# Optimization experiments

Measured on AMD Instinct MI355X. Metric: run time of the kernel, lower is better.

The kernel has to match this reference:

```python
import jax, jax.numpy as jnp
import numpy as np

B, S, H = 32, 2048, 1024

def setup_inputs() -> dict:
    key = jax.random.key(0)
    ks = jax.random.split(key, 8)
    scale = 1.0 / np.sqrt(H)
    return {
        "decoder_hidden": jax.random.normal(ks[0], (B, 1, H), dtype=jnp.float32),
        "encoder_outputs": jax.random.normal(ks[1], (B, S, H), dtype=jnp.float32),
        "coverage": jax.random.uniform(ks[2], (B, S), dtype=jnp.float32),
        "W_enc": jax.random.normal(ks[3], (H, H), dtype=jnp.float32) * scale,  # enc_v.weight [out,in]
        "W_dec": jax.random.normal(ks[4], (H, H), dtype=jnp.float32) * scale,  # dec_v.weight
        "b_dec": jax.random.normal(ks[5], (H,), dtype=jnp.float32) * scale,    # dec_v.bias
        "w_cov": jax.random.normal(ks[6], (H,), dtype=jnp.float32) * scale,    # cov_v.weight [H,1] squeezed
        "v": jax.random.normal(ks[7], (H,), dtype=jnp.float32) * scale,        # V_prime.weight [1,H] squeezed
    }

def reference(decoder_hidden, encoder_outputs, coverage, W_enc, W_dec, b_dec, w_cov, v):
    # enc_feature: [B,S,H]; torch Linear is x @ W.T
    enc_feature = jnp.einsum("bsh,oh->bso", encoder_outputs, W_enc)
    # dec_feature: [B,1,H], broadcasts over S
    dec_feature = jnp.einsum("bqh,oh->bqo", decoder_hidden, W_dec) + b_dec
    # cov_feature: coverage[...,None] @ w_cov[None,:] -> [B,S,H]
    cov_feature = coverage[..., None] * w_cov
    scores = jnp.tanh(enc_feature + dec_feature + cov_feature)  # [B,S,H]
    attn_scores = jnp.einsum("bsh,h->bs", scores, v)            # V_prime, squeeze(-1)
    attn_dist = jax.nn.softmax(attn_scores, axis=-1)[:, None, :]  # [B,1,S]
    return attn_dist
```

## Files before the change

### kernel.cpp

```cpp
#include <hip/hip_runtime.h>
#include <hip/hip_bf16.h>

#define Bb 32
#define Ss 2048
#define Hh 1024

typedef __attribute__((ext_vector_type(4))) float f32x4;
typedef __attribute__((ext_vector_type(8))) short s16x8;

#define GAS const __attribute__((address_space(1))) unsigned int
#define LAS __attribute__((address_space(3))) unsigned int

__device__ __forceinline__ unsigned short f2bf(float x) {
  unsigned int u = __float_as_uint(x);
  u = (u + 0x7fffu + ((u >> 16) & 1u)) >> 16;
  return (unsigned short)u;
}

__global__ void cvt_bf16_kernel(const float* __restrict__ in,
                                unsigned short* __restrict__ out, int n8) {
  int idx = blockIdx.x * blockDim.x + threadIdx.x;
  int stride = gridDim.x * blockDim.x;
  for (int i = idx; i < n8; i += stride) {
    const float4* p = reinterpret_cast<const float4*>(in) + 2 * (size_t)i;
    float4 a = p[0];
    float4 b = p[1];
    union { unsigned short u[8]; uint4 q; } r;
    r.u[0] = f2bf(a.x); r.u[1] = f2bf(a.y); r.u[2] = f2bf(a.z); r.u[3] = f2bf(a.w);
    r.u[4] = f2bf(b.x); r.u[5] = f2bf(b.y); r.u[6] = f2bf(b.z); r.u[7] = f2bf(b.w);
    reinterpret_cast<uint4*>(out)[i] = r.q;
  }
}

__global__ void dec_feat_kernel(const float* __restrict__ dh,
                                const float* __restrict__ Wd,
                                const float* __restrict__ bd,
                                float* __restrict__ out) {
  int gw = blockIdx.x * 4 + (threadIdx.x >> 6);
  int lane = threadIdx.x & 63;
  int b = gw >> 10;
  int o = gw & 1023;
  const float4* x = reinterpret_cast<const float4*>(dh + (size_t)b * Hh);
  const float4* w = reinterpret_cast<const float4*>(Wd + (size_t)o * Hh);
  float acc = 0.f;
#pragma unroll
  for (int it = 0; it < 4; ++it) {
    float4 xa = x[lane + it * 64];
    float4 wa = w[lane + it * 64];
    acc += xa.x * wa.x + xa.y * wa.y + xa.z * wa.z + xa.w * wa.w;
  }
#pragma unroll
  for (int m = 1; m < 64; m <<= 1) acc += __shfl_xor(acc, m, 64);
  if (lane == 0) out[gw] = acc + bd[o];
}

__global__ void __launch_bounds__(256, 2)
gemm_tanh_kernel(const unsigned short* __restrict__ A,
                 const unsigned short* __restrict__ W,
                 const float* __restrict__ decf,
                 const float* __restrict__ cov,
                 const float* __restrict__ wcov,
                 const float* __restrict__ v,
                 float* __restrict__ scores) {
  __shared__ unsigned short lds[2 * 8192];

  int bid = blockIdx.x;
  int swz = (bid & 7) * 512 + (bid >> 3);
  int s_tile = swz >> 3;
  int o_tile = swz & 7;

  const int tid = threadIdx.x;
  const int lane = tid & 63;
  const int wid = tid >> 6;
  const int wr = wid >> 1;
  const int wc = wid & 1;
  const int fr = lane & 15;
  const int fk = (lane >> 4) * 8;

  const size_t a_base = (size_t)s_tile * 128 * 1024;
  const size_t b_base = (size_t)o_tile * 128 * 1024;
  const int st_row = tid >> 2;
  const int st_k = (tid & 3) * 8;
  const unsigned short* gA = A + a_base + (size_t)st_row * 1024 + st_k;
  const unsigned short* gB = W + b_base + (size_t)st_row * 1024 + st_k;
  unsigned short* la = lds + tid * 8;

#define STAGE(buf, kt) do {                                                        \
    const unsigned short* _ga = gA + (size_t)(kt) * 32;                            \
    const unsigned short* _gb = gB + (size_t)(kt) * 32;                            \
    unsigned short* _la = la + (buf) * 8192;                                       \
    __builtin_amdgcn_global_load_lds((GAS*)(_ga),         (LAS*)(_la),        16, 0, 0); \
    __builtin_amdgcn_global_load_lds((GAS*)(_ga + 65536), (LAS*)(_la + 2048), 16, 0, 0); \
    __builtin_amdgcn_global_load_lds((GAS*)(_gb),         (LAS*)(_la + 4096), 16, 0, 0); \
    __builtin_amdgcn_global_load_lds((GAS*)(_gb + 65536), (LAS*)(_la + 6144), 16, 0, 0); \
  } while (0)

  f32x4 acc[4][4];
#pragma unroll
  for (int i = 0; i < 4; ++i)
#pragma unroll
    for (int j = 0; j < 4; ++j) acc[i][j] = (f32x4){0.f, 0.f, 0.f, 0.f};

  STAGE(0, 0);
  __syncthreads();
  int buf = 0;
  const unsigned short* baseA0 = lds + (size_t)(wr * 64 + fr) * 32 + fk;
  const unsigned short* baseB0 = lds + 4096 + (size_t)(wc * 64 + fr) * 32 + fk;

  for (int kt = 0; kt < 32; ++kt) {
    if (kt < 31) STAGE(buf ^ 1, kt + 1);
    const unsigned short* bA = baseA0 + buf * 8192;
    const unsigned short* bB = baseB0 + buf * 8192;
    s16x8 af[4], bfr[4];
#pragma unroll
    for (int i = 0; i < 4; ++i) af[i] = *reinterpret_cast<const s16x8*>(bA + i * 512);
#pragma unroll
    for (int j = 0; j < 4; ++j) bfr[j] = *reinterpret_cast<const s16x8*>(bB + j * 512);
#pragma unroll
    for (int i = 0; i < 4; ++i)
#pragma unroll
      for (int j = 0; j < 4; ++j)
        acc[i][j] = __builtin_amdgcn_mfma_f32_16x16x32_bf16(af[i], bfr[j], acc[i][j], 0, 0, 0);
    __syncthreads();
    buf ^= 1;
  }
#undef STAGE

  const int row_base = s_tile * 128 + wr * 64 + (lane >> 4) * 4;
  const int o_base_g = o_tile * 128 + wc * 64 + fr;
  const int bb = (s_tile * 128) >> 11;

  float vv[4], dv[4], wv[4];
#pragma unroll
  for (int j = 0; j < 4; ++j) {
    int o = o_base_g + j * 16;
    vv[j] = v[o];
    wv[j] = wcov[o];
    dv[j] = decf[bb * 1024 + o];
  }

#pragma unroll
  for (int i = 0; i < 4; ++i) {
#pragma unroll
    for (int r = 0; r < 4; ++r) {
      int s_flat = row_base + i * 16 + r;
      float c = cov[s_flat];
      float sum = 0.f;
#pragma unroll
      for (int j = 0; j < 4; ++j) {
        float x = acc[i][j][r] + dv[j] + c * wv[j];
        sum += tanhf(x) * vv[j];
      }
      sum += __shfl_xor(sum, 1, 64);
      sum += __shfl_xor(sum, 2, 64);
      sum += __shfl_xor(sum, 4, 64);
      sum += __shfl_xor(sum, 8, 64);
      if (fr == 0) atomicAdd(&scores[s_flat], sum);
    }
  }
}

__global__ void softmax_kernel(const float* __restrict__ scores, float* __restrict__ out) {
  int b = blockIdx.x;
  int tid = threadIdx.x;
  int lane = tid & 63, w = tid >> 6;
  const float* row = scores + (size_t)b * Ss;
  float vals[8];
#pragma unroll
  for (int k = 0; k < 8; ++k) vals[k] = row[tid + k * 256];
  float m = vals[0];
#pragma unroll
  for (int k = 1; k < 8; ++k) m = fmaxf(m, vals[k]);
#pragma unroll
  for (int off = 1; off < 64; off <<= 1) m = fmaxf(m, __shfl_xor(m, off, 64));
  __shared__ float sm[4], ss[4];
  if (lane == 0) sm[w] = m;
  __syncthreads();
  m = fmaxf(fmaxf(sm[0], sm[1]), fmaxf(sm[2], sm[3]));
  float s = 0.f;
#pragma unroll
  for (int k = 0; k < 8; ++k) { vals[k] = __expf(vals[k] - m); s += vals[k]; }
#pragma unroll
  for (int off = 1; off < 64; off <<= 1) s += __shfl_xor(s, off, 64);
  if (lane == 0) ss[w] = s;
  __syncthreads();
  s = ss[0] + ss[1] + ss[2] + ss[3];
  float inv = 1.f / s;
#pragma unroll
  for (int k = 0; k < 8; ++k) out[(size_t)b * Ss + tid + k * 256] = vals[k] * inv;
}

extern "C" void kernel_launch(void* const* d_in, const int* in_sizes, int n_in,
                              void* d_out, int out_size, void* d_ws, size_t ws_size,
                              hipStream_t stream) {
  const float* dh    = (const float*)d_in[0];
  const float* enc   = (const float*)d_in[1];
  const float* cov   = (const float*)d_in[2];
  const float* W_enc = (const float*)d_in[3];
  const float* W_dec = (const float*)d_in[4];
  const float* b_dec = (const float*)d_in[5];
  const float* w_cov = (const float*)d_in[6];
  const float* v     = (const float*)d_in[7];
  float* out = (float*)d_out;

  char* ws = (char*)d_ws;
  unsigned short* A_bf  = (unsigned short*)ws;
  unsigned short* W_bf  = (unsigned short*)(ws + 134217728);
  float*          decf  = (float*)(ws + 136314880);
  float*          score = (float*)(ws + 136445952);

  hipMemsetAsync(score, 0, (size_t)Bb * Ss * sizeof(float), stream);
  cvt_bf16_kernel<<<4096, 256, 0, stream>>>(enc, A_bf, (Bb * Ss * Hh) / 8);
  cvt_bf16_kernel<<<512, 256, 0, stream>>>(W_enc, W_bf, (Hh * Hh) / 8);
  dec_feat_kernel<<<(Bb * Hh) / 4, 256, 0, stream>>>(dh, W_dec, b_dec, decf);
  gemm_tanh_kernel<<<4096, 256, 0, stream>>>(A_bf, W_bf, decf, cov, w_cov, v, score);
  softmax_kernel<<<Bb, 256, 0, stream>>>(score, out);
}
```

Before: 282.4 us.

## Fuse fp32-to-bf16 activation conversion into GEMM with larger swizzled tiles

```diff
diff --git a/kernel.cpp b/kernel.cpp
--- a/kernel.cpp
+++ b/kernel.cpp
@@ -17,19 +17,18 @@
   return (unsigned short)u;
 }
 
-__global__ void cvt_bf16_kernel(const float* __restrict__ in,
-                                unsigned short* __restrict__ out, int n8) {
-  int idx = blockIdx.x * blockDim.x + threadIdx.x;
-  int stride = gridDim.x * blockDim.x;
-  for (int i = idx; i < n8; i += stride) {
-    const float4* p = reinterpret_cast<const float4*>(in) + 2 * (size_t)i;
-    float4 a = p[0];
-    float4 b = p[1];
-    union { unsigned short u[8]; uint4 q; } r;
-    r.u[0] = f2bf(a.x); r.u[1] = f2bf(a.y); r.u[2] = f2bf(a.z); r.u[3] = f2bf(a.w);
-    r.u[4] = f2bf(b.x); r.u[5] = f2bf(b.y); r.u[6] = f2bf(b.z); r.u[7] = f2bf(b.w);
-    reinterpret_cast<uint4*>(out)[i] = r.q;
-  }
+__global__ void cvt_w_kernel(const float* __restrict__ W, unsigned short* __restrict__ out) {
+  int g = blockIdx.x * blockDim.x + threadIdx.x;
+  int o = g >> 7;
+  int kc8 = (g & 127) << 3;
+  const float4* src = reinterpret_cast<const float4*>(W + (size_t)o * Hh + kc8);
+  float4 a = src[0], b = src[1];
+  union { unsigned short u[8]; uint4 q; } rr;
+  rr.u[0] = f2bf(a.x); rr.u[1] = f2bf(a.y); rr.u[2] = f2bf(a.z); rr.u[3] = f2bf(a.w);
+  rr.u[4] = f2bf(b.x); rr.u[5] = f2bf(b.y); rr.u[6] = f2bf(b.z); rr.u[7] = f2bf(b.w);
+  int ot = o >> 8, r = o & 255, kt = kc8 >> 6, kc = kc8 & 63;
+  size_t byte = (size_t)(ot * 16 + kt) * 32768 + (size_t)((r * 128 + kc * 2) ^ ((r & 7) << 4));
+  *reinterpret_cast<uint4*>(reinterpret_cast<char*>(out) + byte) = rr.q;
 }
 
 __global__ void dec_feat_kernel(const float* __restrict__ dh,
@@ -54,102 +53,137 @@
   if (lane == 0) out[gw] = acc + bd[o];
 }
 
-__global__ void __launch_bounds__(256, 2)
-gemm_tanh_kernel(const unsigned short* __restrict__ A,
-                 const unsigned short* __restrict__ W,
-                 const float* __restrict__ decf,
-                 const float* __restrict__ cov,
-                 const float* __restrict__ wcov,
-                 const float* __restrict__ v,
-                 float* __restrict__ scores) {
-  __shared__ unsigned short lds[2 * 8192];
+__global__ void __launch_bounds__(512, 2)
+gemm_fused(const float* __restrict__ A,
+           const unsigned short* __restrict__ Bw,
+           const float* __restrict__ decf,
+           const float* __restrict__ cov,
+           const float* __restrict__ wcov,
+           const float* __restrict__ v,
+           float* __restrict__ scores) {
+  __shared__ uint4 lds_v[8192];
+  char* lds = reinterpret_cast<char*>(lds_v);
 
   int bid = blockIdx.x;
-  int swz = (bid & 7) * 512 + (bid >> 3);
-  int s_tile = swz >> 3;
-  int o_tile = swz & 7;
+  int swz = (bid & 7) * 128 + (bid >> 3);
+  const int s_tile = swz >> 2;
+  const int ot = swz & 3;
 
   const int tid = threadIdx.x;
   const int lane = tid & 63;
   const int wid = tid >> 6;
-  const int wr = wid >> 1;
-  const int wc = wid & 1;
-  const int fr = lane & 15;
-  const int fk = (lane >> 4) * 8;
-
-  const size_t a_base = (size_t)s_tile * 128 * 1024;
-  const size_t b_base = (size_t)o_tile * 128 * 1024;
-  const int st_row = tid >> 2;
-  const int st_k = (tid & 3) * 8;
-  const unsigned short* gA = A + a_base + (size_t)st_row * 1024 + st_k;
-  const unsigned short* gB = W + b_base + (size_t)st_row * 1024 + st_k;
-  unsigned short* la = lds + tid * 8;
-
-#define STAGE(buf, kt) do {                                                        \
-    const unsigned short* _ga = gA + (size_t)(kt) * 32;                            \
-    const unsigned short* _gb = gB + (size_t)(kt) * 32;                            \
-    unsigned short* _la = la + (buf) * 8192;                                       \
-    __builtin_amdgcn_global_load_lds((GAS*)(_ga),         (LAS*)(_la),        16, 0, 0); \
-    __builtin_amdgcn_global_load_lds((GAS*)(_ga + 65536), (LAS*)(_la + 2048), 16, 0, 0); \
-    __builtin_amdgcn_global_load_lds((GAS*)(_gb),         (LAS*)(_la + 4096), 16, 0, 0); \
-    __builtin_amdgcn_global_load_lds((GAS*)(_gb + 65536), (LAS*)(_la + 6144), 16, 0, 0); \
-  } while (0)
-
-  f32x4 acc[4][4];
-#pragma unroll
-  for (int i = 0; i < 4; ++i)
+  const int wm = wid >> 2, wn = wid & 3;
+  const int fr = lane & 15, hi = lane >> 4;
+
+  const int arow = tid >> 3, apc = tid & 7;
+  const float* gA = A + (size_t)(s_tile * 256 + arow) * 1024 + apc * 8;
+  const int aswz = (arow & 7) << 4;
+
+  const char* gB = reinterpret_cast<const char*>(Bw) + (size_t)ot * 16 * 32768 + tid * 16;
+
+  const int fswz = (fr & 7) << 4;
+  const int aFragBase = (wm * 128 + fr) * 128 + hi * 16;
+  const int bFragBase = 32768 + (wn * 64 + fr) * 128 + hi * 16;
+
+  f32x4 acc[8][4];
+#pragma unroll
+  for (int i = 0; i < 8; ++i)
 #pragma unroll
     for (int j = 0; j < 4; ++j) acc[i][j] = (f32x4){0.f, 0.f, 0.f, 0.f};
 
-  STAGE(0, 0);
+  float4 sa[4][2];
+
+#define GLOAD_A(kt) do {                                                         \
+    const float* _p = gA + (size_t)(kt) * 64;                                    \
+    _Pragma("unroll") for (int i = 0; i < 4; ++i) {                              \
+      sa[i][0] = *reinterpret_cast<const float4*>(_p + (size_t)i * 65536);       \
+      sa[i][1] = *reinterpret_cast<const float4*>(_p + (size_t)i * 65536 + 4);   \
+    }                                                                            \
+  } while (0)
+
+#define GLOAD_B(kt, b) do {                                                      \
+    _Pragma("unroll") for (int i = 0; i < 4; ++i)                                \
+      __builtin_amdgcn_global_load_lds((GAS*)(gB + (size_t)(kt) * 32768 + i * 8192), \
+          (LAS*)(lds + (b) * 65536 + 32768 + i * 8192 + tid * 16), 16, 0, 0);    \
+  } while (0)
+
+#define AWRITE(b) do {                                                           \
+    _Pragma("unroll") for (int i = 0; i < 4; ++i) {                              \
+      union { unsigned short u[8]; uint4 q; } w;                                 \
+      float4 x = sa[i][0], y = sa[i][1];                                         \
+      w.u[0] = f2bf(x.x); w.u[1] = f2bf(x.y); w.u[2] = f2bf(x.z); w.u[3] = f2bf(x.w); \
+      w.u[4] = f2bf(y.x); w.u[5] = f2bf(y.y); w.u[6] = f2bf(y.z); w.u[7] = f2bf(y.w); \
+      int _byte = (((i * 64 + arow) * 128 + apc * 16) ^ aswz);                   \
+      *reinterpret_cast<uint4*>(lds + (b) * 65536 + _byte) = w.q;                \
+    }                                                                            \
+  } while (0)
+
+#define COMPUTE(b) do {                                                          \
+    const char* Lb = lds + (b) * 65536;                                          \
+    s16x8 bfr[4][2];                                                             \
+    _Pragma("unroll") for (int fn = 0; fn < 4; ++fn)                             \
+      _Pragma("unroll") for (int ks = 0; ks < 2; ++ks)                           \
+        bfr[fn][ks] = *reinterpret_cast<const s16x8*>(                           \
+            Lb + ((bFragBase + fn * 2048 + ks * 64) ^ fswz));                    \
+    _Pragma("unroll") for (int mh = 0; mh < 2; ++mh) {                           \
+      s16x8 af[4][2];                                                            \
+      _Pragma("unroll") for (int fm = 0; fm < 4; ++fm)                           \
+        _Pragma("unroll") for (int ks = 0; ks < 2; ++ks)                         \
+          af[fm][ks] = *reinterpret_cast<const s16x8*>(                          \
+              Lb + ((aFragBase + (mh * 4 + fm) * 2048 + ks * 64) ^ fswz));       \
+      _Pragma("unroll") for (int fm = 0; fm < 4; ++fm)                           \
+        _Pragma("unroll") for (int fn = 0; fn < 4; ++fn)                         \
+          _Pragma("unroll") for (int ks = 0; ks < 2; ++ks)                       \
+            acc[mh * 4 + fm][fn] = __builtin_amdgcn_mfma_f32_16x16x32_bf16(      \
+                af[fm][ks], bfr[fn][ks], acc[mh * 4 + fm][fn], 0, 0, 0);         \
+    }                                                                            \
+  } while (0)
+
+  GLOAD_A(0);
+  GLOAD_B(0, 0);
+  AWRITE(0);
   __syncthreads();
-  int buf = 0;
-  const unsigned short* baseA0 = lds + (size_t)(wr * 64 + fr) * 32 + fk;
-  const unsigned short* baseB0 = lds + 4096 + (size_t)(wc * 64 + fr) * 32 + fk;
-
-  for (int kt = 0; kt < 32; ++kt) {
-    if (kt < 31) STAGE(buf ^ 1, kt + 1);
-    const unsigned short* bA = baseA0 + buf * 8192;
-    const unsigned short* bB = baseB0 + buf * 8192;
-    s16x8 af[4], bfr[4];
-#pragma unroll
-    for (int i = 0; i < 4; ++i) af[i] = *reinterpret_cast<const s16x8*>(bA + i * 512);
-#pragma unroll
-    for (int j = 0; j < 4; ++j) bfr[j] = *reinterpret_cast<const s16x8*>(bB + j * 512);
-#pragma unroll
-    for (int i = 0; i < 4; ++i)
-#pragma unroll
-      for (int j = 0; j < 4; ++j)
-        acc[i][j] = __builtin_amdgcn_mfma_f32_16x16x32_bf16(af[i], bfr[j], acc[i][j], 0, 0, 0);
+
+  for (int t = 0; t < 16; ++t) {
+    int b = t & 1;
+    if (t < 15) {
+      GLOAD_A(t + 1);
+      GLOAD_B(t + 1, b ^ 1);
+    }
+    COMPUTE(b);
+    if (t < 15) AWRITE(b ^ 1);
     __syncthreads();
-    buf ^= 1;
-  }
-#undef STAGE
-
-  const int row_base = s_tile * 128 + wr * 64 + (lane >> 4) * 4;
-  const int o_base_g = o_tile * 128 + wc * 64 + fr;
-  const int bb = (s_tile * 128) >> 11;
-
-  float vv[4], dv[4], wv[4];
-#pragma unroll
-  for (int j = 0; j < 4; ++j) {
-    int o = o_base_g + j * 16;
-    vv[j] = v[o];
-    wv[j] = wcov[o];
-    dv[j] = decf[bb * 1024 + o];
-  }
-
-#pragma unroll
-  for (int i = 0; i < 4; ++i) {
+  }
+
+#undef GLOAD_A
+#undef GLOAD_B
+#undef AWRITE
+#undef COMPUTE
+
+  const int row0 = s_tile * 256 + wm * 128 + hi * 4;
+  const int o0 = ot * 256 + wn * 64 + fr;
+  const int bb = s_tile >> 3;
+
+  float vv[4], wv[4], dv[4];
+#pragma unroll
+  for (int fn = 0; fn < 4; ++fn) {
+    int o = o0 + fn * 16;
+    vv[fn] = v[o];
+    wv[fn] = wcov[o];
+    dv[fn] = decf[bb * 1024 + o];
+  }
+
+#pragma unroll
+  for (int fm = 0; fm < 8; ++fm) {
 #pragma unroll
     for (int r = 0; r < 4; ++r) {
-      int s_flat = row_base + i * 16 + r;
+      int s_flat = row0 + fm * 16 + r;
       float c = cov[s_flat];
       float sum = 0.f;
 #pragma unroll
-      for (int j = 0; j < 4; ++j) {
-        float x = acc[i][j][r] + dv[j] + c * wv[j];
-        sum += tanhf(x) * vv[j];
+      for (int fn = 0; fn < 4; ++fn) {
+        float x = acc[fm][fn][r] + dv[fn] + c * wv[fn];
+        sum += tanhf(x) * vv[fn];
       }
       sum += __shfl_xor(sum, 1, 64);
       sum += __shfl_xor(sum, 2, 64);
@@ -204,15 +238,13 @@
   float* out = (float*)d_out;
 
   char* ws = (char*)d_ws;
-  unsigned short* A_bf  = (unsigned short*)ws;
-  unsigned short* W_bf  = (unsigned short*)(ws + 134217728);
-  float*          decf  = (float*)(ws + 136314880);
-  float*          score = (float*)(ws + 136445952);
+  unsigned short* Wswz = (unsigned short*)ws;
+  float*          decf = (float*)(ws + 2097152);
+  float*          score = (float*)(ws + 2097152 + 131072);
 
   hipMemsetAsync(score, 0, (size_t)Bb * Ss * sizeof(float), stream);
-  cvt_bf16_kernel<<<4096, 256, 0, stream>>>(enc, A_bf, (Bb * Ss * Hh) / 8);
-  cvt_bf16_kernel<<<512, 256, 0, stream>>>(W_enc, W_bf, (Hh * Hh) / 8);
+  cvt_w_kernel<<<512, 256, 0, stream>>>(W_enc, Wswz);
   dec_feat_kernel<<<(Bb * Hh) / 4, 256, 0, stream>>>(dh, W_dec, b_dec, decf);
-  gemm_tanh_kernel<<<4096, 256, 0, stream>>>(A_bf, W_bf, decf, cov, w_cov, v, score);
+  gemm_fused<<<1024, 512, 0, stream>>>(enc, Wswz, decf, cov, w_cov, v, score);
   softmax_kernel<<<Bb, 256, 0, stream>>>(score, out);
 }
```

Result: slower. 290.5 us (+2.9%).
